# Optimization experiments

Hardware: AMD Instinct MI355X
Metric: run time of the kernel (lower is better)

Reference implementation:

```python
import jax, jax.numpy as jnp
import numpy as np
from jax import lax

R = 20        # box-filter radius
NITERS = 5    # mean-field iterations


def _box1d(x, r):
    # box filter of radius r along the last axis, via cumsum (integral image)
    n = x.shape[-1]
    cs = jnp.cumsum(x, axis=-1)
    upper = jnp.concatenate([cs[..., r:], jnp.repeat(cs[..., -1:], r, axis=-1)], axis=-1)
    lower = jnp.concatenate([jnp.zeros_like(cs[..., : r + 1]), cs[..., : n - r - 1]], axis=-1)
    return upper - lower


def _box(x, r):
    # 2D box filter over the last two axes
    x = _box1d(x, r)
    x = _box1d(jnp.swapaxes(x, -1, -2), r)
    return jnp.swapaxes(x, -1, -2)


def _guided_filter(p, I, eps, r):
    # He et al. color guided filter: filter p [B,L,H,W] guided by I [B,C,H,W]
    B, C, H, W = I.shape
    Nrm = _box(jnp.ones((H, W), p.dtype), r)          # [H,W] window counts
    mI = _box(I, r) / Nrm                              # [B,C,H,W]
    mp = _box(p, r) / Nrm                              # [B,L,H,W]
    corr_Ip = _box(I[:, :, None] * p[:, None], r) / Nrm    # [B,C,L,H,W]
    cov_Ip = corr_Ip - mI[:, :, None] * mp[:, None]
    corr_II = _box(I[:, :, None] * I[:, None], r) / Nrm    # [B,C,C,H,W]
    var_I = corr_II - mI[:, :, None] * mI[:, None]
    A = var_I + eps * jnp.eye(C, dtype=p.dtype)[None, :, :, None, None]
    # per-pixel CxC solve: move matrix dims last
    A_ = jnp.transpose(A, (0, 3, 4, 1, 2))             # [B,H,W,C,C]
    rhs = jnp.transpose(cov_Ip, (0, 3, 4, 1, 2))       # [B,H,W,C,L]
    a = jnp.linalg.solve(A_, rhs)                      # [B,H,W,C,L]
    a = jnp.transpose(a, (0, 3, 4, 1, 2))              # [B,C,L,H,W]
    b = mp - jnp.einsum('bclhw,bchw->blhw', a, mI)     # [B,L,H,W]
    q = jnp.einsum('bclhw,bchw->blhw', _box(a, r) / Nrm, I) + _box(b, r) / Nrm
    return q


def setup_inputs() -> dict:
    key = jax.random.key(0)
    k1, k2 = jax.random.split(key)
    B, L, C, H, W = 2, 21, 3, 512, 512
    E0 = jax.random.normal(k1, (B, L, H, W), dtype=jnp.float32)
    Refs = jax.random.uniform(k2, (B, C, H, W), dtype=jnp.float32)
    # Potts-initialized 1x1 conv weight: ones minus identity
    W_mu = jnp.ones((L, L), jnp.float32) - jnp.eye(L, dtype=jnp.float32)
    eps = jnp.full((1,), 1e-5, dtype=jnp.float32)
    return {"E0": E0, "Refs": Refs, "W_mu": W_mu, "eps": eps}


def reference(E0, Refs, W_mu, eps):
    e = eps[0]
    Q0 = jax.nn.softmax(-E0, axis=1)

    def step(Q, _):
        MuQ = jnp.einsum('lm,bmhw->blhw', W_mu, Q)     # 1x1 conv, no bias
        E = E0 + _guided_filter(MuQ, Refs, e, R)
        Q = jax.nn.softmax(-E, axis=1)
        return Q, None

    Q, _ = lax.scan(step, Q0, None, length=NITERS)
    return Q
```

## Files before the change

### kernel.cpp

```cpp
#include <hip/hip_runtime.h>
#include <hip/hip_bf16.h>

typedef _Float16 f16;
typedef _Float16 f16v2 __attribute__((ext_vector_type(2)));
typedef _Float16 f16v4 __attribute__((ext_vector_type(4)));
typedef _Float16 f16v8 __attribute__((ext_vector_type(8)));

#define BB   2
#define LL   21
#define HH   512
#define WW   512
#define RR   20
#define NCH  84
#define HW   (HH*WW)
#define VSEG 64

#define WROW 576
#define RSTR 2320
#define NSTRIP 6
#define NGRP 11

__device__ __forceinline__ float nrminv(int x, int y) {
    int cx = min(x + RR, WW - 1) - max(x - RR, 0) + 1;
    int cy = min(y + RR, HH - 1) - max(y - RR, 0) + 1;
    return 1.0f / (float)(cx * cy);
}

__device__ __forceinline__ int swz(int w) { return w ^ ((w >> 3) & 0x1C); }

__global__ __launch_bounds__(128) void vboxf_k(const float* __restrict__ src,
                                               float* __restrict__ dst) {
    int pp = blockIdx.y;
    int y0 = blockIdx.x * VSEG;
    const float* s = src + (size_t)pp * HW + threadIdx.x * 4;
    float* d = dst + (size_t)pp * HW + threadIdx.x * 4;
    float s0 = 0.f, s1 = 0.f, s2 = 0.f, s3 = 0.f;
    int lo = y0 - RR; if (lo < 0) lo = 0;
    int hi = y0 + RR;
    for (int yy = lo; yy <= hi; ++yy) {
        float4 v = *(const float4*)(s + (size_t)yy * WW);
        s0 += v.x; s1 += v.y; s2 += v.z; s3 += v.w;
    }
    { float4 o = {s0, s1, s2, s3}; *(float4*)(d + (size_t)y0 * WW) = o; }
    #pragma unroll 4
    for (int y = y0 + 1; y < y0 + VSEG; ++y) {
        int ya = y + RR, ys = y - RR - 1;
        if (ya < HH) {
            float4 v = *(const float4*)(s + (size_t)ya * WW);
            s0 += v.x; s1 += v.y; s2 += v.z; s3 += v.w;
        }
        if (ys >= 0) {
            float4 v = *(const float4*)(s + (size_t)ys * WW);
            s0 -= v.x; s1 -= v.y; s2 -= v.z; s3 -= v.w;
        }
        float4 o = {s0, s1, s2, s3};
        *(float4*)(d + (size_t)y * WW) = o;
    }
}

template <typename T, typename V4>
__device__ __forceinline__ void load_win16(const T* __restrict__ srow, int x0,
                                           float* __restrict__ raw) {
    #pragma unroll
    for (int c = 0; c < 15; ++c) {
        int st = x0 - 24 + 4 * c;
        if (st >= 0 && st < WW) {
            V4 v = *(const V4*)(srow + st);
            raw[4*c+0] = (float)v.x; raw[4*c+1] = (float)v.y;
            raw[4*c+2] = (float)v.z; raw[4*c+3] = (float)v.w;
        } else {
            raw[4*c+0] = 0.f; raw[4*c+1] = 0.f; raw[4*c+2] = 0.f; raw[4*c+3] = 0.f;
        }
    }
}
__device__ __forceinline__ void slide16(const float* __restrict__ raw,
                                        float* __restrict__ res) {
    float sum = 0.f;
    #pragma unroll
    for (int j = 4; j <= 44; ++j) sum += raw[j];
    res[0] = sum;
    #pragma unroll
    for (int k = 1; k < 16; ++k) { sum += raw[k+44] - raw[k+3]; res[k] = sum; }
}

__global__ __launch_bounds__(256) void hboxf_k(const float* __restrict__ src,
                                               float* __restrict__ dst) {
    int pp = blockIdx.y;
    int row = blockIdx.x * 8 + (threadIdx.x >> 5);
    int x0 = (threadIdx.x & 31) << 4;
    const float* srow = src + (size_t)pp * HW + (size_t)row * WW;
    float raw[60], res[16];
    load_win16<float, float4>(srow, x0, raw);
    slide16(raw, res);
    float* drow = dst + (size_t)pp * HW + (size_t)row * WW + x0;
    #pragma unroll
    for (int g = 0; g < 4; ++g) {
        float4 o = {res[4*g], res[4*g+1], res[4*g+2], res[4*g+3]};
        *(float4*)(drow + 4*g) = o;
    }
}

__device__ __forceinline__ void produce8(const f16* __restrict__ pu,
                                         float* __restrict__ ldsrow0,
                                         float* __restrict__ va,
                                         int gy, int yend, int buf,
                                         int ws0, int ws1) {
    #pragma unroll
    for (int k = 0; k < 8; ++k) {
        int y = gy + k;
        if (y < yend) {
            int ya = y + RR;
            if (ya < HH) {
                f16v8 v = *(const f16v8*)(pu + (size_t)ya * WW);
                #pragma unroll
                for (int i = 0; i < 8; ++i) va[i] += (float)v[i];
            }
            int yb = y - RR - 1;
            if (yb >= 0) {
                f16v8 v = *(const f16v8*)(pu + (size_t)yb * WW);
                #pragma unroll
                for (int i = 0; i < 8; ++i) va[i] -= (float)v[i];
            }
            float* dst = ldsrow0 + (size_t)(buf * 8 + k) * RSTR;
            float4 a = {va[0], va[1], va[2], va[3]};
            float4 b4 = {va[4], va[5], va[6], va[7]};
            *(float4*)(dst + ws0) = a;
            *(float4*)(dst + ws1) = b4;
        }
    }
}

__device__ __forceinline__ void load_raw_lds(const float* __restrict__ base,
                                             int x0, float* __restrict__ raw) {
    #pragma unroll
    for (int k = 0; k < 16; ++k) {
        int w = x0 + 4 * k;
        float4 v = *(const float4*)(base + swz(w));
        raw[4*k+0] = v.x; raw[4*k+1] = v.y; raw[4*k+2] = v.z; raw[4*k+3] = v.w;
    }
}

__device__ __forceinline__ void zero_pads(float* __restrict__ lds) {
    for (int p = threadIdx.x; p < 16 * 4 * 64; p += 512) {
        int ringrow = p >> 8;
        int rem = p & 255;
        int chp = rem >> 6, j = rem & 63;
        int w = (j < 24) ? j : (512 + j);
        lds[(size_t)ringrow * RSTR + chp * WROW + swz(w)] = 0.f;
    }
}

__global__ __launch_bounds__(512, 2) void fused_solve_k(const f16* __restrict__ U,
                                                        f16* __restrict__ V,
                                                        const float* __restrict__ Ainv,
                                                        const float* __restrict__ mI) {
    __shared__ float lds[16 * RSTR];
    int bl = blockIdx.y;
    int b = bl / LL, l = bl - b * LL;
    int strip = blockIdx.x;
    int y0s = (strip * HH) / NSTRIP;
    int yend = ((strip + 1) * HH) / NSTRIP;
    bool prod = (threadIdx.x < 256);

    int pch = threadIdx.x >> 6;
    int cx = (threadIdx.x & 63) * 8;
    int chsel = (pch == 0) ? l : (LL + (pch - 1) * LL + l);
    const f16* pu = U + (size_t)(b * NCH + chsel) * HW + cx;
    float* ldsrow0 = lds + pch * WROW;
    int ws0 = swz(cx + 24);
    int ws1 = swz(cx + 28);
    float va[8];
    #pragma unroll
    for (int i = 0; i < 8; ++i) va[i] = 0.f;

    zero_pads(lds);

    if (prod) {
        int lo = y0s - RR - 1; if (lo < 0) lo = 0;
        for (int yy = lo; yy <= y0s + RR - 1; ++yy) {
            f16v8 v = *(const f16v8*)(pu + (size_t)yy * WW);
            #pragma unroll
            for (int i = 0; i < 8; ++i) va[i] += (float)v[i];
        }
        produce8(pu, ldsrow0, va, y0s, yend, 0, ws0, ws1);
    }
    __syncthreads();

    int u = threadIdx.x - 256;
    int r = u >> 5, i = u & 31;
    int x0 = i << 4;

    for (int g = 1; g <= NGRP; ++g) {
        if (prod) {
            if (g < NGRP) produce8(pu, ldsrow0, va, y0s + g * 8, yend, g & 1, ws0, ws1);
        } else {
            int gc = g - 1;
            int row = y0s + gc * 8 + r;
            if (row < yend) {
                float res[4][16];
                const float* rbase = lds + (size_t)((gc & 1) * 8 + r) * RSTR;
                #pragma unroll
                for (int c = 0; c < 4; ++c) {
                    float raw[64];
                    load_raw_lds(rbase + c * WROW, x0, raw);
                    slide16(raw, res[c]);
                }
                size_t pixb = (size_t)row * WW + x0;
                size_t ab = (size_t)b * 6 * HW + pixb;
                size_t mb = (size_t)b * 3 * HW + pixb;
                #pragma unroll
                for (int gq = 0; gq < 4; ++gq) {
                    float iv[6][4], mi[3][4];
                    #pragma unroll
                    for (int j = 0; j < 6; ++j) {
                        float4 v = *(const float4*)(Ainv + ab + (size_t)j * HW + 4 * gq);
                        iv[j][0] = v.x; iv[j][1] = v.y; iv[j][2] = v.z; iv[j][3] = v.w;
                    }
                    #pragma unroll
                    for (int j = 0; j < 3; ++j) {
                        float4 v = *(const float4*)(mI + mb + (size_t)j * HW + 4 * gq);
                        mi[j][0] = v.x; mi[j][1] = v.y; mi[j][2] = v.z; mi[j][3] = v.w;
                    }
                    #pragma unroll
                    for (int e = 0; e < 4; ++e) {
                        int k = 4 * gq + e;
                        float nrm = nrminv(x0 + k, row);
                        float mp   = res[0][k] * nrm;
                        float cov0 = res[1][k] * nrm - mi[0][e] * mp;
                        float cov1 = res[2][k] * nrm - mi[1][e] * mp;
                        float cov2 = res[3][k] * nrm - mi[2][e] * mp;
                        float a0 = iv[0][e] * cov0 + iv[1][e] * cov1 + iv[2][e] * cov2;
                        float a1 = iv[1][e] * cov0 + iv[3][e] * cov1 + iv[4][e] * cov2;
                        float a2 = iv[2][e] * cov0 + iv[4][e] * cov1 + iv[5][e] * cov2;
                        float bb = mp - (a0 * mi[0][e] + a1 * mi[1][e] + a2 * mi[2][e]);
                        res[0][k] = bb; res[1][k] = a0; res[2][k] = a1; res[3][k] = a2;
                    }
                }
                #pragma unroll
                for (int c = 0; c < 4; ++c) {
                    int chx = (c == 0) ? l : (LL + (c - 1) * LL + l);
                    f16* drow = V + (size_t)(b * NCH + chx) * HW + pixb;
                    f16v8 o0, o1;
                    #pragma unroll
                    for (int e = 0; e < 8; ++e) { o0[e] = (f16)res[c][e]; o1[e] = (f16)res[c][8+e]; }
                    *(f16v8*)(drow) = o0;
                    *(f16v8*)(drow + 8) = o1;
                }
            }
        }
        if (g < NGRP) __syncthreads();
    }
}

__global__ __launch_bounds__(512, 2) void fused_q_k(const f16* __restrict__ V,
                                                    const float* __restrict__ Refs,
                                                    f16* __restrict__ Q) {
    __shared__ float lds[16 * RSTR];
    int bl = blockIdx.y;
    int b = bl / LL, l = bl - b * LL;
    int strip = blockIdx.x;
    int y0s = (strip * HH) / NSTRIP;
    int yend = ((strip + 1) * HH) / NSTRIP;
    bool prod = (threadIdx.x < 256);

    int pch = threadIdx.x >> 6;
    int cx = (threadIdx.x & 63) * 8;
    int chsel = (pch == 0) ? l : (LL + (pch - 1) * LL + l);
    const f16* pu = V + (size_t)(b * NCH + chsel) * HW + cx;
    float* ldsrow0 = lds + pch * WROW;
    int ws0 = swz(cx + 24);
    int ws1 = swz(cx + 28);
    float va[8];
    #pragma unroll
    for (int i = 0; i < 8; ++i) va[i] = 0.f;

    zero_pads(lds);

    if (prod) {
        int lo = y0s - RR - 1; if (lo < 0) lo = 0;
        for (int yy = lo; yy <= y0s + RR - 1; ++yy) {
            f16v8 v = *(const f16v8*)(pu + (size_t)yy * WW);
            #pragma unroll
            for (int i = 0; i < 8; ++i) va[i] += (float)v[i];
        }
        produce8(pu, ldsrow0, va, y0s, yend, 0, ws0, ws1);
    }
    __syncthreads();

    int u = threadIdx.x - 256;
    int r = u >> 5, i = u & 31;
    int x0 = i << 4;

    for (int g = 1; g <= NGRP; ++g) {
        if (prod) {
            if (g < NGRP) produce8(pu, ldsrow0, va, y0s + g * 8, yend, g & 1, ws0, ws1);
        } else {
            int gc = g - 1;
            int row = y0s + gc * 8 + r;
            if (row < yend) {
                float res[4][16];
                const float* rbase = lds + (size_t)((gc & 1) * 8 + r) * RSTR;
                #pragma unroll
                for (int c = 0; c < 4; ++c) {
                    float raw[64];
                    load_raw_lds(rbase + c * WROW, x0, raw);
                    slide16(raw, res[c]);
                }
                size_t pixb = (size_t)row * WW + x0;
                f16* qrow = Q + (size_t)(b * LL + l) * HW + pixb;
                f16 tmpo[16];
                #pragma unroll
                for (int gq = 0; gq < 4; ++gq) {
                    float4 i0 = *(const float4*)(Refs + ((size_t)b * 3 + 0) * HW + pixb + 4 * gq);
                    float4 i1 = *(const float4*)(Refs + ((size_t)b * 3 + 1) * HW + pixb + 4 * gq);
                    float4 i2 = *(const float4*)(Refs + ((size_t)b * 3 + 2) * HW + pixb + 4 * gq);
                    float ic0[4] = {i0.x, i0.y, i0.z, i0.w};
                    float ic1[4] = {i1.x, i1.y, i1.z, i1.w};
                    float ic2[4] = {i2.x, i2.y, i2.z, i2.w};
                    #pragma unroll
                    for (int e = 0; e < 4; ++e) {
                        int k = 4 * gq + e;
                        float nrm = nrminv(x0 + k, row);
                        float q = (res[0][k] + res[1][k] * ic0[e] + res[2][k] * ic1[e]
                                   + res[3][k] * ic2[e]) * nrm;
                        tmpo[k] = (f16)q;
                    }
                }
                f16v8 o0, o1;
                #pragma unroll
                for (int e = 0; e < 8; ++e) { o0[e] = tmpo[e]; o1[e] = tmpo[8+e]; }
                *(f16v8*)(qrow) = o0;
                *(f16v8*)(qrow + 8) = o1;
            }
        }
        if (g < NGRP) __syncthreads();
    }
}

__global__ __launch_bounds__(256) void prod_k(float* __restrict__ Pf,
                                              const float* __restrict__ Refs) {
    int idx = blockIdx.x * 256 + threadIdx.x;
    int b = idx >> 18, pix = idx & (HW - 1);
    float I0 = Refs[((size_t)b * 3 + 0) * HW + pix];
    float I1 = Refs[((size_t)b * 3 + 1) * HW + pix];
    float I2 = Refs[((size_t)b * 3 + 2) * HW + pix];
    size_t base = (size_t)b * 9 * HW + pix;
    Pf[base + (size_t)0 * HW] = I0;
    Pf[base + (size_t)1 * HW] = I1;
    Pf[base + (size_t)2 * HW] = I2;
    Pf[base + (size_t)3 * HW] = I0 * I0;
    Pf[base + (size_t)4 * HW] = I0 * I1;
    Pf[base + (size_t)5 * HW] = I0 * I2;
    Pf[base + (size_t)6 * HW] = I1 * I1;
    Pf[base + (size_t)7 * HW] = I1 * I2;
    Pf[base + (size_t)8 * HW] = I2 * I2;
}

__global__ __launch_bounds__(256) void prep_k(const float* __restrict__ Bf,
                                              float* __restrict__ Ainv, float* __restrict__ mI,
                                              const float* __restrict__ epsp) {
    int idx = blockIdx.x * 256 + threadIdx.x;
    int b = idx >> 18, pix = idx & (HW - 1);
    int x = pix & (WW - 1), y = pix >> 9;
    float nrm = nrminv(x, y);
    float eps = epsp[0];
    size_t base = (size_t)b * 9 * HW + pix;
    float m0 = Bf[base + (size_t)0 * HW] * nrm;
    float m1 = Bf[base + (size_t)1 * HW] * nrm;
    float m2 = Bf[base + (size_t)2 * HW] * nrm;
    float v00 = Bf[base + (size_t)3 * HW] * nrm - m0 * m0 + eps;
    float v01 = Bf[base + (size_t)4 * HW] * nrm - m0 * m1;
    float v02 = Bf[base + (size_t)5 * HW] * nrm - m0 * m2;
    float v11 = Bf[base + (size_t)6 * HW] * nrm - m1 * m1 + eps;
    float v12 = Bf[base + (size_t)7 * HW] * nrm - m1 * m2;
    float v22 = Bf[base + (size_t)8 * HW] * nrm - m2 * m2 + eps;
    float c00 = v11 * v22 - v12 * v12;
    float c01 = v02 * v12 - v01 * v22;
    float c02 = v01 * v12 - v02 * v11;
    float c11 = v00 * v22 - v02 * v02;
    float c12 = v01 * v02 - v00 * v12;
    float c22 = v00 * v11 - v01 * v01;
    float det = v00 * c00 + v01 * c01 + v02 * c02;
    float id = 1.0f / det;
    size_t ab = (size_t)b * 6 * HW + pix;
    Ainv[ab + (size_t)0 * HW] = c00 * id;
    Ainv[ab + (size_t)1 * HW] = c01 * id;
    Ainv[ab + (size_t)2 * HW] = c02 * id;
    Ainv[ab + (size_t)3 * HW] = c11 * id;
    Ainv[ab + (size_t)4 * HW] = c12 * id;
    Ainv[ab + (size_t)5 * HW] = c22 * id;
    size_t mb = (size_t)b * 3 * HW + pix;
    mI[mb]                  = m0;
    mI[mb + (size_t)HW]     = m1;
    mI[mb + (size_t)2 * HW] = m2;
}

__global__ __launch_bounds__(256) void e_k(const f16* __restrict__ Q,
                                           f16* __restrict__ pout,
                                           const float* __restrict__ E0,
                                           const float* __restrict__ Refs,
                                           const float* __restrict__ Wf,
                                           float* __restrict__ out, int mode) {
    int idx = blockIdx.x * 256 + threadIdx.x;
    int b = idx >> 17;
    int pix = (idx & (HW / 2 - 1)) * 2;
    size_t base  = (size_t)b * NCH * HW + pix;
    size_t ebase = (size_t)b * LL * HW + pix;
    float2 Ic0 = *(const float2*)(Refs + ((size_t)b * 3 + 0) * HW + pix);
    float2 Ic1 = *(const float2*)(Refs + ((size_t)b * 3 + 1) * HW + pix);
    float2 Ic2 = *(const float2*)(Refs + ((size_t)b * 3 + 2) * HW + pix);
    float Ev0[LL], Ev1[LL];
    float m0 = -1e30f, m1 = -1e30f;
    #pragma unroll
    for (int l = 0; l < LL; ++l) {
        float2 e0 = *(const float2*)(E0 + ebase + (size_t)l * HW);
        float v0 = e0.x, v1 = e0.y;
        if (mode != 0) {
            f16v2 qv = *(const f16v2*)(Q + ebase + (size_t)l * HW);
            v0 += (float)qv.x; v1 += (float)qv.y;
        }
        Ev0[l] = -v0; Ev1[l] = -v1;
        m0 = fmaxf(m0, Ev0[l]); m1 = fmaxf(m1, Ev1[l]);
    }
    float s0 = 0.f, s1 = 0.f;
    #pragma unroll
    for (int l = 0; l < LL; ++l) {
        Ev0[l] = __expf(Ev0[l] - m0); s0 += Ev0[l];
        Ev1[l] = __expf(Ev1[l] - m1); s1 += Ev1[l];
    }
    float i0 = 1.0f / s0, i1 = 1.0f / s1;
    if (mode == 2) {
        #pragma unroll
        for (int l = 0; l < LL; ++l) {
            float2 o; o.x = Ev0[l] * i0; o.y = Ev1[l] * i1;
            *(float2*)(out + ebase + (size_t)l * HW) = o;
        }
    } else {
        #pragma unroll
        for (int l = 0; l < LL; ++l) { Ev0[l] *= i0; Ev1[l] *= i1; }
        #pragma unroll
        for (int l = 0; l < LL; ++l) {
            float p0 = 0.f, p1 = 0.f;
            #pragma unroll
            for (int m = 0; m < LL; ++m) {
                float w = Wf[l * LL + m];
                p0 += w * Ev0[m]; p1 += w * Ev1[m];
            }
            f16v2 o;
            o.x = (f16)p0; o.y = (f16)p1;
            *(f16v2*)(pout + base + (size_t)l * HW) = o;
            o.x = (f16)(p0 * Ic0.x); o.y = (f16)(p1 * Ic0.y);
            *(f16v2*)(pout + base + (size_t)(LL + 0*LL + l) * HW) = o;
            o.x = (f16)(p0 * Ic1.x); o.y = (f16)(p1 * Ic1.y);
            *(f16v2*)(pout + base + (size_t)(LL + 1*LL + l) * HW) = o;
            o.x = (f16)(p0 * Ic2.x); o.y = (f16)(p1 * Ic2.y);
            *(f16v2*)(pout + base + (size_t)(LL + 2*LL + l) * HW) = o;
        }
    }
}

extern "C" void kernel_launch(void* const* d_in, const int* in_sizes, int n_in,
                              void* d_out, int out_size, void* d_ws, size_t ws_size,
                              hipStream_t stream) {
    const float* E0   = (const float*)d_in[0];
    const float* Refs = (const float*)d_in[1];
    const float* Wmu  = (const float*)d_in[2];
    const float* epsp = (const float*)d_in[3];
    float* out = (float*)d_out;

    size_t Ub = (size_t)BB * NCH * HW * 2;
    size_t Ab = (size_t)BB * 6 * HW * 4;
    size_t Mb = (size_t)BB * 3 * HW * 4;
    char* ws = (char*)d_ws;
    f16*   U    = (f16*)ws;
    f16*   V    = (f16*)(ws + Ub);
    float* Ainv = (float*)(ws + 2 * Ub);
    float* mI   = (float*)(ws + 2 * Ub + Ab);
    f16*   Qb   = (f16*)(ws + 2 * Ub + Ab + Mb);
    float* Uf   = (float*)U;
    float* Vf   = (float*)V;

    int nblk = (BB * HW) / 256;
    prod_k<<<nblk, 256, 0, stream>>>(Uf, Refs);
    vboxf_k<<<dim3(HH / VSEG, BB * 9), 128, 0, stream>>>(Uf, Vf);
    hboxf_k<<<dim3(HH / 8, BB * 9), 256, 0, stream>>>(Vf, Uf);
    prep_k<<<nblk, 256, 0, stream>>>(Uf, Ainv, mI, epsp);
    e_k<<<(BB * HW / 2) / 256, 256, 0, stream>>>(Qb, U, E0, Refs, Wmu, out, 0);

    for (int t = 1; t <= 5; ++t) {
        fused_solve_k<<<dim3(NSTRIP, BB * LL), 512, 0, stream>>>(U, V, Ainv, mI);
        fused_q_k<<<dim3(NSTRIP, BB * LL), 512, 0, stream>>>(V, Refs, Qb);
        e_k<<<(BB * HW / 2) / 256, 256, 0, stream>>>(Qb, U, E0, Refs, Wmu, out,
                                                     t == 5 ? 2 : 1);
    }
}
```

Before: 1.219 ms.

## Store vertical box sums in fp16 LDS ring to raise occupancy and remap block order

The LDS ring holding vertically summed rows now stores fp16 chunks instead of fp32, halving shared memory per block. Launch bounds move from 2 to 4 blocks per CU. The grid is flattened so consecutive blocks cover different planes of the same strip, padded to 48 planes with early exit. This trades extra precision loss in the intermediate box sums and conversion work for more occupancy and possibly better L2 locality.

```diff
diff --git a/kernel.cpp b/kernel.cpp
--- a/kernel.cpp
+++ b/kernel.cpp
@@ -15,10 +15,12 @@
 #define HW   (HH*WW)
 #define VSEG 64
 
-#define WROW 576
-#define RSTR 2320
+#define CHUNKS_CH 72
+#define ROWCHUNKS 288
+#define RROW_F16  2312
 #define NSTRIP 6
 #define NGRP 11
+#define NPLANE 48
 
 __device__ __forceinline__ float nrminv(int x, int y) {
     int cx = min(x + RR, WW - 1) - max(x - RR, 0) + 1;
@@ -26,7 +28,7 @@
     return 1.0f / (float)(cx * cy);
 }
 
-__device__ __forceinline__ int swz(int w) { return w ^ ((w >> 3) & 0x1C); }
+__device__ __forceinline__ int swzc(int c) { return c ^ ((c >> 3) & 7); }
 
 __global__ __launch_bounds__(128) void vboxf_k(const float* __restrict__ src,
                                                float* __restrict__ dst) {
@@ -101,10 +103,9 @@
 }
 
 __device__ __forceinline__ void produce8(const f16* __restrict__ pu,
-                                         float* __restrict__ ldsrow0,
+                                         f16* __restrict__ ring,
                                          float* __restrict__ va,
-                                         int gy, int yend, int buf,
-                                         int ws0, int ws1) {
+                                         int gy, int yend, int buf, int coff) {
     #pragma unroll
     for (int k = 0; k < 8; ++k) {
         int y = gy + k;
@@ -121,59 +122,59 @@
                 #pragma unroll
                 for (int i = 0; i < 8; ++i) va[i] -= (float)v[i];
             }
-            float* dst = ldsrow0 + (size_t)(buf * 8 + k) * RSTR;
-            float4 a = {va[0], va[1], va[2], va[3]};
-            float4 b4 = {va[4], va[5], va[6], va[7]};
-            *(float4*)(dst + ws0) = a;
-            *(float4*)(dst + ws1) = b4;
-        }
-    }
-}
-
-__device__ __forceinline__ void load_raw_lds(const float* __restrict__ base,
-                                             int x0, float* __restrict__ raw) {
-    #pragma unroll
-    for (int k = 0; k < 16; ++k) {
-        int w = x0 + 4 * k;
-        float4 v = *(const float4*)(base + swz(w));
-        raw[4*k+0] = v.x; raw[4*k+1] = v.y; raw[4*k+2] = v.z; raw[4*k+3] = v.w;
-    }
-}
-
-__device__ __forceinline__ void zero_pads(float* __restrict__ lds) {
-    for (int p = threadIdx.x; p < 16 * 4 * 64; p += 512) {
-        int ringrow = p >> 8;
-        int rem = p & 255;
-        int chp = rem >> 6, j = rem & 63;
-        int w = (j < 24) ? j : (512 + j);
-        lds[(size_t)ringrow * RSTR + chp * WROW + swz(w)] = 0.f;
-    }
-}
-
-__global__ __launch_bounds__(512, 2) void fused_solve_k(const f16* __restrict__ U,
+            f16v8 o;
+            #pragma unroll
+            for (int i = 0; i < 8; ++i) o[i] = (f16)va[i];
+            *(f16v8*)(ring + (size_t)(buf * 8 + k) * RROW_F16 + coff) = o;
+        }
+    }
+}
+
+__device__ __forceinline__ void load_raw16(const f16* __restrict__ rrow,
+                                           int ch, int i, float* __restrict__ raw) {
+    int cb = ch * CHUNKS_CH + 2 * i;
+    #pragma unroll
+    for (int cc = 0; cc < 8; ++cc) {
+        f16v8 v = *(const f16v8*)(rrow + 8 * swzc(cb + cc));
+        #pragma unroll
+        for (int e = 0; e < 8; ++e) raw[8*cc+e] = (float)v[e];
+    }
+}
+
+__device__ __forceinline__ void zero_pads16(f16* __restrict__ ring) {
+    int tid = threadIdx.x;
+    int rr = tid >> 5, rem = tid & 31;
+    int ch = rem >> 3, k = rem & 7;
+    int cic = (k < 3) ? k : (64 + k);
+    f16v8 z = {};
+    *(f16v8*)(ring + (size_t)rr * RROW_F16 + 8 * swzc(ch * CHUNKS_CH + cic)) = z;
+}
+
+__global__ __launch_bounds__(512, 4) void fused_solve_k(const f16* __restrict__ U,
                                                         f16* __restrict__ V,
                                                         const float* __restrict__ Ainv,
                                                         const float* __restrict__ mI) {
-    __shared__ float lds[16 * RSTR];
-    int bl = blockIdx.y;
-    int b = bl / LL, l = bl - b * LL;
-    int strip = blockIdx.x;
+    __shared__ f16 ring[16 * RROW_F16];
+    int id = blockIdx.x;
+    int plane = id % NPLANE;
+    int strip = id / NPLANE;
+    if (plane >= 2 * LL) return;
+    int b = plane & 1, l = plane >> 1;
     int y0s = (strip * HH) / NSTRIP;
     int yend = ((strip + 1) * HH) / NSTRIP;
     bool prod = (threadIdx.x < 256);
 
     int pch = threadIdx.x >> 6;
-    int cx = (threadIdx.x & 63) * 8;
+    int lanec = threadIdx.x & 63;
+    int cx = lanec * 8;
     int chsel = (pch == 0) ? l : (LL + (pch - 1) * LL + l);
     const f16* pu = U + (size_t)(b * NCH + chsel) * HW + cx;
-    float* ldsrow0 = lds + pch * WROW;
-    int ws0 = swz(cx + 24);
-    int ws1 = swz(cx + 28);
+    int coff = 8 * swzc(pch * CHUNKS_CH + lanec + 3);
     float va[8];
     #pragma unroll
     for (int i = 0; i < 8; ++i) va[i] = 0.f;
 
-    zero_pads(lds);
+    zero_pads16(ring);
 
     if (prod) {
         int lo = y0s - RR - 1; if (lo < 0) lo = 0;
@@ -182,7 +183,7 @@
             #pragma unroll
             for (int i = 0; i < 8; ++i) va[i] += (float)v[i];
         }
-        produce8(pu, ldsrow0, va, y0s, yend, 0, ws0, ws1);
+        produce8(pu, ring, va, y0s, yend, 0, coff);
     }
     __syncthreads();
 
@@ -192,17 +193,17 @@
 
     for (int g = 1; g <= NGRP; ++g) {
         if (prod) {
-            if (g < NGRP) produce8(pu, ldsrow0, va, y0s + g * 8, yend, g & 1, ws0, ws1);
+            if (g < NGRP) produce8(pu, ring, va, y0s + g * 8, yend, g & 1, coff);
         } else {
             int gc = g - 1;
             int row = y0s + gc * 8 + r;
             if (row < yend) {
                 float res[4][16];
-                const float* rbase = lds + (size_t)((gc & 1) * 8 + r) * RSTR;
+                const f16* rrow = ring + (size_t)((gc & 1) * 8 + r) * RROW_F16;
                 #pragma unroll
                 for (int c = 0; c < 4; ++c) {
                     float raw[64];
-                    load_raw_lds(rbase + c * WROW, x0, raw);
+                    load_raw16(rrow, c, i, raw);
                     slide16(raw, res[c]);
                 }
                 size_t pixb = (size_t)row * WW + x0;
@@ -252,29 +253,30 @@
     }
 }
 
-__global__ __launch_bounds__(512, 2) void fused_q_k(const f16* __restrict__ V,
+__global__ __launch_bounds__(512, 4) void fused_q_k(const f16* __restrict__ V,
                                                     const float* __restrict__ Refs,
                                                     f16* __restrict__ Q) {
-    __shared__ float lds[16 * RSTR];
-    int bl = blockIdx.y;
-    int b = bl / LL, l = bl - b * LL;
-    int strip = blockIdx.x;
+    __shared__ f16 ring[16 * RROW_F16];
+    int id = blockIdx.x;
+    int plane = id % NPLANE;
+    int strip = id / NPLANE;
+    if (plane >= 2 * LL) return;
+    int b = plane & 1, l = plane >> 1;
     int y0s = (strip * HH) / NSTRIP;
     int yend = ((strip + 1) * HH) / NSTRIP;
     bool prod = (threadIdx.x < 256);
 
     int pch = threadIdx.x >> 6;
-    int cx = (threadIdx.x & 63) * 8;
+    int lanec = threadIdx.x & 63;
+    int cx = lanec * 8;
     int chsel = (pch == 0) ? l : (LL + (pch - 1) * LL + l);
     const f16* pu = V + (size_t)(b * NCH + chsel) * HW + cx;
-    float* ldsrow0 = lds + pch * WROW;
-    int ws0 = swz(cx + 24);
-    int ws1 = swz(cx + 28);
+    int coff = 8 * swzc(pch * CHUNKS_CH + lanec + 3);
     float va[8];
     #pragma unroll
     for (int i = 0; i < 8; ++i) va[i] = 0.f;
 
-    zero_pads(lds);
+    zero_pads16(ring);
 
     if (prod) {
         int lo = y0s - RR - 1; if (lo < 0) lo = 0;
@@ -283,7 +285,7 @@
             #pragma unroll
             for (int i = 0; i < 8; ++i) va[i] += (float)v[i];
         }
-        produce8(pu, ldsrow0, va, y0s, yend, 0, ws0, ws1);
+        produce8(pu, ring, va, y0s, yend, 0, coff);
     }
     __syncthreads();
 
@@ -293,17 +295,17 @@
 
     for (int g = 1; g <= NGRP; ++g) {
         if (prod) {
-            if (g < NGRP) produce8(pu, ldsrow0, va, y0s + g * 8, yend, g & 1, ws0, ws1);
+            if (g < NGRP) produce8(pu, ring, va, y0s + g * 8, yend, g & 1, coff);
         } else {
             int gc = g - 1;
             int row = y0s + gc * 8 + r;
             if (row < yend) {
                 float res[4][16];
-                const float* rbase = lds + (size_t)((gc & 1) * 8 + r) * RSTR;
+                const f16* rrow = ring + (size_t)((gc & 1) * 8 + r) * RROW_F16;
                 #pragma unroll
                 for (int c = 0; c < 4; ++c) {
                     float raw[64];
-                    load_raw_lds(rbase + c * WROW, x0, raw);
+                    load_raw16(rrow, c, i, raw);
                     slide16(raw, res[c]);
                 }
                 size_t pixb = (size_t)row * WW + x0;
@@ -488,8 +490,8 @@
     e_k<<<(BB * HW / 2) / 256, 256, 0, stream>>>(Qb, U, E0, Refs, Wmu, out, 0);
 
     for (int t = 1; t <= 5; ++t) {
-        fused_solve_k<<<dim3(NSTRIP, BB * LL), 512, 0, stream>>>(U, V, Ainv, mI);
-        fused_q_k<<<dim3(NSTRIP, BB * LL), 512, 0, stream>>>(V, Refs, Qb);
+        fused_solve_k<<<NPLANE * NSTRIP, 512, 0, stream>>>(U, V, Ainv, mI);
+        fused_q_k<<<NPLANE * NSTRIP, 512, 0, stream>>>(V, Refs, Qb);
         e_k<<<(BB * HW / 2) / 256, 256, 0, stream>>>(Qb, U, E0, Refs, Wmu, out,
                                                      t == 5 ? 2 : 1);
     }
```

Result: slower. 3.191 ms (+161.8%).

## Halve LDS ring and per-thread tile, double strips for higher occupancy

Applied to the files above, without the earlier changes.

The fused solve and Q kernels now use more, shorter strips. Producers fill 4 rows per group instead of 8, and consumer threads each compute 8 pixels instead of 16. This halves the LDS ring from 16 to 8 rows, which lets more blocks fit per CU and launches twice as many blocks. It also cuts consumer register pressure by shrinking the raw and result arrays. In exchange, each strip repeats the vertical prefix accumulation, and each output needs more overlapping window loads from LDS.

```diff
diff --git a/kernel.cpp b/kernel.cpp
--- a/kernel.cpp
+++ b/kernel.cpp
@@ -17,7 +17,9 @@
 
 #define WROW 576
 #define RSTR 2320
-#define NSTRIP 6
+#define NRING 8
+#define GRP 4
+#define NSTRIP 12
 #define NGRP 11
 
 __device__ __forceinline__ float nrminv(int x, int y) {
@@ -82,6 +84,15 @@
     #pragma unroll
     for (int k = 1; k < 16; ++k) { sum += raw[k+44] - raw[k+3]; res[k] = sum; }
 }
+__device__ __forceinline__ void slide8(const float* __restrict__ raw,
+                                       float* __restrict__ res) {
+    float sum = 0.f;
+    #pragma unroll
+    for (int j = 4; j <= 44; ++j) sum += raw[j];
+    res[0] = sum;
+    #pragma unroll
+    for (int k = 1; k < 8; ++k) { sum += raw[k+44] - raw[k+3]; res[k] = sum; }
+}
 
 __global__ __launch_bounds__(256) void hboxf_k(const float* __restrict__ src,
                                                float* __restrict__ dst) {
@@ -100,13 +111,13 @@
     }
 }
 
-__device__ __forceinline__ void produce8(const f16* __restrict__ pu,
+__device__ __forceinline__ void produce4(const f16* __restrict__ pu,
                                          float* __restrict__ ldsrow0,
                                          float* __restrict__ va,
                                          int gy, int yend, int buf,
                                          int ws0, int ws1) {
     #pragma unroll
-    for (int k = 0; k < 8; ++k) {
+    for (int k = 0; k < GRP; ++k) {
         int y = gy + k;
         if (y < yend) {
             int ya = y + RR;
@@ -121,7 +132,7 @@
                 #pragma unroll
                 for (int i = 0; i < 8; ++i) va[i] -= (float)v[i];
             }
-            float* dst = ldsrow0 + (size_t)(buf * 8 + k) * RSTR;
+            float* dst = ldsrow0 + (size_t)(buf * GRP + k) * RSTR;
             float4 a = {va[0], va[1], va[2], va[3]};
             float4 b4 = {va[4], va[5], va[6], va[7]};
             *(float4*)(dst + ws0) = a;
@@ -130,10 +141,10 @@
     }
 }
 
-__device__ __forceinline__ void load_raw_lds(const float* __restrict__ base,
-                                             int x0, float* __restrict__ raw) {
-    #pragma unroll
-    for (int k = 0; k < 16; ++k) {
+__device__ __forceinline__ void load_raw8(const float* __restrict__ base,
+                                          int x0, float* __restrict__ raw) {
+    #pragma unroll
+    for (int k = 0; k < 14; ++k) {
         int w = x0 + 4 * k;
         float4 v = *(const float4*)(base + swz(w));
         raw[4*k+0] = v.x; raw[4*k+1] = v.y; raw[4*k+2] = v.z; raw[4*k+3] = v.w;
@@ -141,7 +152,7 @@
 }
 
 __device__ __forceinline__ void zero_pads(float* __restrict__ lds) {
-    for (int p = threadIdx.x; p < 16 * 4 * 64; p += 512) {
+    for (int p = threadIdx.x; p < NRING * 4 * 64; p += 512) {
         int ringrow = p >> 8;
         int rem = p & 255;
         int chp = rem >> 6, j = rem & 63;
@@ -154,7 +165,7 @@
                                                         f16* __restrict__ V,
                                                         const float* __restrict__ Ainv,
                                                         const float* __restrict__ mI) {
-    __shared__ float lds[16 * RSTR];
+    __shared__ float lds[NRING * RSTR];
     int bl = blockIdx.y;
     int b = bl / LL, l = bl - b * LL;
     int strip = blockIdx.x;
@@ -182,34 +193,35 @@
             #pragma unroll
             for (int i = 0; i < 8; ++i) va[i] += (float)v[i];
         }
-        produce8(pu, ldsrow0, va, y0s, yend, 0, ws0, ws1);
+        produce4(pu, ldsrow0, va, y0s, yend, 0, ws0, ws1);
     }
     __syncthreads();
 
     int u = threadIdx.x - 256;
-    int r = u >> 5, i = u & 31;
-    int x0 = i << 4;
+    int r = u >> 6, i = u & 63;
+    int x0 = i << 3;
 
     for (int g = 1; g <= NGRP; ++g) {
         if (prod) {
-            if (g < NGRP) produce8(pu, ldsrow0, va, y0s + g * 8, yend, g & 1, ws0, ws1);
+            if (g < NGRP) produce4(pu, ldsrow0, va, y0s + g * GRP, yend, g & 1, ws0, ws1);
         } else {
             int gc = g - 1;
-            int row = y0s + gc * 8 + r;
+            int row = y0s + gc * GRP + r;
             if (row < yend) {
-                float res[4][16];
-                const float* rbase = lds + (size_t)((gc & 1) * 8 + r) * RSTR;
+                float res[4][8];
+                const float* rbase = lds + (size_t)((gc & 1) * GRP + r) * RSTR;
                 #pragma unroll
                 for (int c = 0; c < 4; ++c) {
-                    float raw[64];
-                    load_raw_lds(rbase + c * WROW, x0, raw);
-                    slide16(raw, res[c]);
+                    float raw[56];
+                    load_raw8(rbase + c * WROW, x0, raw);
+                    slide8(raw, res[c]);
                 }
                 size_t pixb = (size_t)row * WW + x0;
                 size_t ab = (size_t)b * 6 * HW + pixb;
                 size_t mb = (size_t)b * 3 * HW + pixb;
-                #pragma unroll
-                for (int gq = 0; gq < 4; ++gq) {
+                f16v8 ob[4];
+                #pragma unroll
+                for (int gq = 0; gq < 2; ++gq) {
                     float iv[6][4], mi[3][4];
                     #pragma unroll
                     for (int j = 0; j < 6; ++j) {
@@ -233,18 +245,14 @@
                         float a1 = iv[1][e] * cov0 + iv[3][e] * cov1 + iv[4][e] * cov2;
                         float a2 = iv[2][e] * cov0 + iv[4][e] * cov1 + iv[5][e] * cov2;
                         float bb = mp - (a0 * mi[0][e] + a1 * mi[1][e] + a2 * mi[2][e]);
-                        res[0][k] = bb; res[1][k] = a0; res[2][k] = a1; res[3][k] = a2;
+                        ob[0][k] = (f16)bb; ob[1][k] = (f16)a0;
+                        ob[2][k] = (f16)a1; ob[3][k] = (f16)a2;
                     }
                 }
                 #pragma unroll
                 for (int c = 0; c < 4; ++c) {
                     int chx = (c == 0) ? l : (LL + (c - 1) * LL + l);
-                    f16* drow = V + (size_t)(b * NCH + chx) * HW + pixb;
-                    f16v8 o0, o1;
-                    #pragma unroll
-                    for (int e = 0; e < 8; ++e) { o0[e] = (f16)res[c][e]; o1[e] = (f16)res[c][8+e]; }
-                    *(f16v8*)(drow) = o0;
-                    *(f16v8*)(drow + 8) = o1;
+                    *(f16v8*)(V + (size_t)(b * NCH + chx) * HW + pixb) = ob[c];
                 }
             }
         }
@@ -255,7 +263,7 @@
 __global__ __launch_bounds__(512, 2) void fused_q_k(const f16* __restrict__ V,
                                                     const float* __restrict__ Refs,
                                                     f16* __restrict__ Q) {
-    __shared__ float lds[16 * RSTR];
+    __shared__ float lds[NRING * RSTR];
     int bl = blockIdx.y;
     int b = bl / LL, l = bl - b * LL;
     int strip = blockIdx.x;
@@ -283,34 +291,33 @@
             #pragma unroll
             for (int i = 0; i < 8; ++i) va[i] += (float)v[i];
         }
-        produce8(pu, ldsrow0, va, y0s, yend, 0, ws0, ws1);
+        produce4(pu, ldsrow0, va, y0s, yend, 0, ws0, ws1);
     }
     __syncthreads();
 
     int u = threadIdx.x - 256;
-    int r = u >> 5, i = u & 31;
-    int x0 = i << 4;
+    int r = u >> 6, i = u & 63;
+    int x0 = i << 3;
 
     for (int g = 1; g <= NGRP; ++g) {
         if (prod) {
-            if (g < NGRP) produce8(pu, ldsrow0, va, y0s + g * 8, yend, g & 1, ws0, ws1);
+            if (g < NGRP) produce4(pu, ldsrow0, va, y0s + g * GRP, yend, g & 1, ws0, ws1);
         } else {
             int gc = g - 1;
-            int row = y0s + gc * 8 + r;
+            int row = y0s + gc * GRP + r;
             if (row < yend) {
-                float res[4][16];
-                const float* rbase = lds + (size_t)((gc & 1) * 8 + r) * RSTR;
+                float res[4][8];
+                const float* rbase = lds + (size_t)((gc & 1) * GRP + r) * RSTR;
                 #pragma unroll
                 for (int c = 0; c < 4; ++c) {
-                    float raw[64];
-                    load_raw_lds(rbase + c * WROW, x0, raw);
-                    slide16(raw, res[c]);
+                    float raw[56];
+                    load_raw8(rbase + c * WROW, x0, raw);
+                    slide8(raw, res[c]);
                 }
                 size_t pixb = (size_t)row * WW + x0;
-                f16* qrow = Q + (size_t)(b * LL + l) * HW + pixb;
-                f16 tmpo[16];
-                #pragma unroll
-                for (int gq = 0; gq < 4; ++gq) {
+                f16v8 o;
+                #pragma unroll
+                for (int gq = 0; gq < 2; ++gq) {
                     float4 i0 = *(const float4*)(Refs + ((size_t)b * 3 + 0) * HW + pixb + 4 * gq);
                     float4 i1 = *(const float4*)(Refs + ((size_t)b * 3 + 1) * HW + pixb + 4 * gq);
                     float4 i2 = *(const float4*)(Refs + ((size_t)b * 3 + 2) * HW + pixb + 4 * gq);
@@ -323,14 +330,10 @@
                         float nrm = nrminv(x0 + k, row);
                         float q = (res[0][k] + res[1][k] * ic0[e] + res[2][k] * ic1[e]
                                    + res[3][k] * ic2[e]) * nrm;
-                        tmpo[k] = (f16)q;
+                        o[k] = (f16)q;
                     }
                 }
-                f16v8 o0, o1;
-                #pragma unroll
-                for (int e = 0; e < 8; ++e) { o0[e] = tmpo[e]; o1[e] = tmpo[8+e]; }
-                *(f16v8*)(qrow) = o0;
-                *(f16v8*)(qrow + 8) = o1;
+                *(f16v8*)(Q + (size_t)(b * LL + l) * HW + pixb) = o;
             }
         }
         if (g < NGRP) __syncthreads();
```

Result: slower. 1.292 ms (+6.0%).
